# Performance work log

Hardware: AMD Instinct MI355X
Metric: run time of the kernel (lower is better)

## Reference

```python
import jax, jax.numpy as jnp
import numpy as np

HEADS = 4
K = 3  # neighborhood kernel size
EPS = 1e-5


def _nbr_idx(dim, k):
    # NATTEN semantics: window start clamped so the full k-window stays in-bounds.
    i = jnp.arange(dim)
    start = jnp.clip(i - k // 2, 0, dim - k)
    return start[:, None] + jnp.arange(k)[None, :]  # [dim, k]


def _gather_windows(t, ix, iy, iz):
    # t: [B, X, Y, Z, n, c] -> [B, X, Y, Z, K^3, n, c]
    t = t[:, ix]                 # [B, X, k, Y, Z, n, c]
    t = t[:, :, :, iy]           # [B, X, k, Y, k, Z, n, c]
    t = t[:, :, :, :, :, iz]     # [B, X, k, Y, k, Z, k, n, c]
    t = t.transpose(0, 1, 3, 5, 2, 4, 6, 7, 8)  # [B,X,Y,Z,k,k,k,n,c]
    B, X, Y, Z = t.shape[0], t.shape[1], t.shape[2], t.shape[3]
    return t.reshape(B, X, Y, Z, K * K * K, HEADS, -1)


def setup_inputs() -> dict:
    key = jax.random.key(0)
    k1, k2, k3 = jax.random.split(key, 3)
    C = 128
    x = jax.random.normal(k1, (1, C, 32, 32, 32), dtype=jnp.float32)
    ln_gamma = jnp.ones((C,), jnp.float32)
    ln_beta = jnp.zeros((C,), jnp.float32)
    qkv_w = jax.random.normal(k2, (3 * C, C), dtype=jnp.float32) * 0.02
    qkv_b = jnp.zeros((3 * C,), jnp.float32)
    proj_w = jax.random.normal(k3, (C, C), dtype=jnp.float32) * 0.02
    proj_b = jnp.zeros((C,), jnp.float32)
    return {"x": x, "ln_gamma": ln_gamma, "ln_beta": ln_beta,
            "qkv_w": qkv_w, "qkv_b": qkv_b, "proj_w": proj_w, "proj_b": proj_b}


def reference(x, ln_gamma, ln_beta, qkv_w, qkv_b, proj_w, proj_b):
    B, C, X, Y, Z = x.shape
    hd = C // HEADS
    scale = hd ** -0.5

    # permute to channels-last + LayerNorm over C
    h = x.transpose(0, 2, 3, 4, 1)  # [B,X,Y,Z,C]
    mu = jnp.mean(h, axis=-1, keepdims=True)
    var = jnp.mean(jnp.square(h - mu), axis=-1, keepdims=True)
    h = (h - mu) * jax.lax.rsqrt(var + EPS) * ln_gamma + ln_beta

    # QKV projection
    qkv = h @ qkv_w.T + qkv_b                     # [B,X,Y,Z,3C]
    q, k, v = jnp.split(qkv, 3, axis=-1)
    q = q.reshape(B, X, Y, Z, HEADS, hd)
    k = k.reshape(B, X, Y, Z, HEADS, hd)
    v = v.reshape(B, X, Y, Z, HEADS, hd)

    ix, iy, iz = _nbr_idx(X, K), _nbr_idx(Y, K), _nbr_idx(Z, K)
    k_win = _gather_windows(k, ix, iy, iz)  # [B,X,Y,Z,27,n,hd]
    v_win = _gather_windows(v, ix, iy, iz)

    attn = jnp.einsum('bxyznc,bxyzknc->bxyznk', q * scale, k_win)
    attn = jax.nn.softmax(attn, axis=-1)
    out = jnp.einsum('bxyznk,bxyzknc->bxyznc', attn, v_win)
    out = out.reshape(B, X, Y, Z, C)

    out = out @ proj_w.T + proj_b                 # output projection
    return out.transpose(0, 4, 1, 2, 3) + x      # residual, channels-first
```

## Files before the change

kernel.cpp:

```cpp
#include <hip/hip_runtime.h>

#define N_VOX 32768
#define CCH 128
#define EPSV 1e-5f

typedef __attribute__((ext_vector_type(8))) short bfrag;
typedef __attribute__((ext_vector_type(4))) float ffrag;
typedef __attribute__((ext_vector_type(2))) unsigned int u32x2;

__device__ __forceinline__ float bf2f(unsigned short u) {
    union { unsigned int i; float f; } c; c.i = ((unsigned int)u) << 16; return c.f;
}
__device__ __forceinline__ unsigned short f2bf(float f) {
    union { float f; unsigned int i; } c; c.f = f;
    unsigned int i = c.i;
    return (unsigned short)((i + 0x7FFFu + ((i >> 16) & 1u)) >> 16);
}
__device__ __forceinline__ unsigned int cvtpk(float lo, float hi) {
    unsigned int r;
    asm("v_cvt_pk_bf16_f32 %0, %1, %2" : "=v"(r) : "v"(lo), "v"(hi));
    return r;
}

__global__ __launch_bounds__(256) void ln_qkv(const float* __restrict__ x,
                                              const float* __restrict__ gamma,
                                              const float* __restrict__ beta,
                                              const float* __restrict__ w,
                                              const float* __restrict__ bias,
                                              unsigned short* __restrict__ qkv) {
    __shared__ __align__(16) unsigned short a_s[64 * 136];
    __shared__ __align__(16) unsigned short b_s[64 * 136];
    __shared__ float ps[256], pq[256];
    __shared__ float muS[64], rsS[64];
    __shared__ float g[128], bta[128];
    int t = threadIdx.x;
    int og = blockIdx.x;
    int v0 = blockIdx.y * 64;
    if (t < 128) { g[t] = gamma[t]; bta[t] = beta[t]; }
    int cq = t >> 6, v = t & 63;
    float xr[32];
    float s = 0.f, sq = 0.f;
    #pragma unroll
    for (int i = 0; i < 32; i++) {
        float val = x[(size_t)(cq * 32 + i) * N_VOX + v0 + v];
        xr[i] = val; s += val; sq += val * val;
    }
    ps[t] = s; pq[t] = sq;
    __syncthreads();
    if (t < 64) {
        float S = ps[t] + ps[t + 64] + ps[t + 128] + ps[t + 192];
        float Q = pq[t] + pq[t + 64] + pq[t + 128] + pq[t + 192];
        float mu = S * (1.0f / 128.0f);
        float var = Q * (1.0f / 128.0f) - mu * mu;
        muS[t] = mu; rsS[t] = rsqrtf(var + EPSV);
    }
    __syncthreads();
    {
        float mu = muS[v], rs = rsS[v];
        #pragma unroll
        for (int i8 = 0; i8 < 4; i8++) {
            float val[8];
            #pragma unroll
            for (int k = 0; k < 8; k++) {
                int c = cq * 32 + i8 * 8 + k;
                val[k] = (xr[i8 * 8 + k] - mu) * rs * g[c] + bta[c];
            }
            uint4 q;
            q.x = cvtpk(val[0], val[1]);
            q.y = cvtpk(val[2], val[3]);
            q.z = cvtpk(val[4], val[5]);
            q.w = cvtpk(val[6], val[7]);
            *(uint4*)&a_s[v * 136 + cq * 32 + i8 * 8] = q;
        }
    }
    __syncthreads();
    int lane = t & 63, wvi = t >> 6, m = lane & 15, quad = lane >> 4;
    bfrag areg[4];
    #pragma unroll
    for (int kk = 0; kk < 4; kk++)
        areg[kk] = *(bfrag*)&a_s[(wvi * 16 + m) * 136 + kk * 32 + quad * 8];
    for (int t0 = 0; t0 < 3; t0++) {
        int o0 = og * 192 + t0 * 64;
        {
            int r4 = t >> 4, c8 = t & 15;
            #pragma unroll
            for (int pass = 0; pass < 4; pass++) {
                int r = pass * 16 + r4;
                float4 w0 = *(const float4*)&w[(size_t)(o0 + r) * 128 + c8 * 8];
                float4 w1 = *(const float4*)&w[(size_t)(o0 + r) * 128 + c8 * 8 + 4];
                uint4 q;
                q.x = cvtpk(w0.x, w0.y);
                q.y = cvtpk(w0.z, w0.w);
                q.z = cvtpk(w1.x, w1.y);
                q.w = cvtpk(w1.z, w1.w);
                *(uint4*)&b_s[r * 136 + c8 * 8] = q;
            }
        }
        __syncthreads();
        ffrag acc[4] = {ffrag{0,0,0,0}, ffrag{0,0,0,0}, ffrag{0,0,0,0}, ffrag{0,0,0,0}};
        #pragma unroll
        for (int kk = 0; kk < 4; kk++) {
            #pragma unroll
            for (int nt = 0; nt < 4; nt++) {
                bfrag bb = *(bfrag*)&b_s[(nt * 16 + m) * 136 + kk * 32 + quad * 8];
                acc[nt] = __builtin_amdgcn_mfma_f32_16x16x32_bf16(areg[kk], bb, acc[nt], 0, 0, 0);
            }
        }
        bool isq = (o0 < 128);
        #pragma unroll
        for (int nt = 0; nt < 4; nt++) {
            int o = o0 + nt * 16 + m;
            float bs = bias[o];
            int sec = o >> 7;
            int oc = o & 127;
            unsigned short* dst = qkv + (size_t)sec * ((size_t)N_VOX * 128);
            #pragma unroll
            for (int r = 0; r < 4; r++) {
                int vg = v0 + wvi * 16 + quad * 4 + r;
                float val = acc[nt][r] + bs;
                if (isq) val *= 0.17677669529663687f;
                dst[(size_t)vg * 128 + oc] = f2bf(val);
            }
        }
        __syncthreads();
    }
}

#define VT2 100
__global__ __launch_bounds__(256) void attn_kernel(const unsigned short* __restrict__ qb,
                                                   const unsigned short* __restrict__ kb,
                                                   const unsigned short* __restrict__ vb,
                                                   unsigned short* __restrict__ ob) {
    __shared__ unsigned int vjtab[96];
    __shared__ __align__(16) unsigned int vmsk[96];
    __shared__ __align__(16) unsigned short vt[4][32 * VT2];

    int t = threadIdx.x;
    int hw = blockIdx.x;
    int bidx = (hw & 7) * 256 + (hw >> 3);
    int czi = bidx & 7, cyi = (bidx >> 3) & 15, cxi = bidx >> 7;
    int cx0 = cxi << 1, cy0 = cyi << 1, cz0 = czi << 2;
    int rx0 = min(max(cx0 - 1, 0), 28);
    int ry0 = min(max(cy0 - 1, 0), 28);
    int rz0 = min(max(cz0 - 1, 0), 26);

    if (t < 96) {
        int r = t;
        int ax = r / 24;
        int rem = r - ax * 24;
        int by = rem / 6;
        int cz = rem - by * 6;
        vjtab[t] = (unsigned)(((rx0 + ax) << 10) + ((ry0 + by) << 5) + (rz0 + cz));
        int wx0 = min(max(cx0 - 1, 0), 29) - rx0;
        int wx1 = min(cx0, 29) - rx0;
        int wy0 = min(max(cy0 - 1, 0), 29) - ry0;
        int wy1 = min(cy0, 29) - ry0;
        unsigned zn = 0;
        #pragma unroll
        for (int vz = 0; vz < 4; vz++) {
            int wz = min(max(cz0 + vz - 1, 0), 29) - rz0;
            if ((unsigned)(cz - wz) <= 2u) zn |= 1u << vz;
        }
        bool x0 = (unsigned)(ax - wx0) <= 2u;
        bool x1 = (unsigned)(ax - wx1) <= 2u;
        bool y0 = (unsigned)(by - wy0) <= 2u;
        bool y1 = (unsigned)(by - wy1) <= 2u;
        unsigned msk = 0;
        if (x0 && y0) msk |= zn;
        if (x0 && y1) msk |= zn << 4;
        if (x1 && y0) msk |= zn << 8;
        if (x1 && y1) msk |= zn << 12;
        vmsk[t] = msk;
    }
    __syncthreads();

    int wave = t >> 6, lane = t & 63;
    int hq = lane >> 4;
    int m = lane & 15;
    int ch0 = wave * 32;

    unsigned short* vts = &vt[wave][0];
    {
        const int cp = m;
        #pragma unroll
        for (int u = 0; u < 6; u++) {
            int rb = u * 16 + hq * 4;
            unsigned int j0 = vjtab[rb + 0];
            unsigned int j1 = vjtab[rb + 1];
            unsigned int j2 = vjtab[rb + 2];
            unsigned int j3 = vjtab[rb + 3];
            unsigned int d0 = *(const unsigned int*)&vb[(size_t)j0 * 128 + ch0 + cp * 2];
            unsigned int d1 = *(const unsigned int*)&vb[(size_t)j1 * 128 + ch0 + cp * 2];
            unsigned int d2 = *(const unsigned int*)&vb[(size_t)j2 * 128 + ch0 + cp * 2];
            unsigned int d3 = *(const unsigned int*)&vb[(size_t)j3 * 128 + ch0 + cp * 2];
            unsigned int lo01 = __builtin_amdgcn_perm(d1, d0, 0x05040100u);
            unsigned int lo23 = __builtin_amdgcn_perm(d3, d2, 0x05040100u);
            unsigned int hi01 = __builtin_amdgcn_perm(d1, d0, 0x07060302u);
            unsigned int hi23 = __builtin_amdgcn_perm(d3, d2, 0x07060302u);
            u32x2 wlo; wlo.x = lo01; wlo.y = lo23;
            u32x2 whi; whi.x = hi01; whi.y = hi23;
            *(u32x2*)&vts[(2 * cp) * VT2 + rb] = wlo;
            *(u32x2*)&vts[(2 * cp + 1) * VT2 + rb] = whi;
        }
    }

    int gx = cx0 + (m >> 3), gy = cy0 + ((m >> 2) & 1), gz = cz0 + (m & 3);
    int vox = (gx << 10) + (gy << 5) + gz;

    bfrag qf = *(const bfrag*)&qb[(size_t)vox * 128 + ch0 + hq * 8];
    ffrag s[6];
    #pragma unroll
    for (int f = 0; f < 6; f++) {
        unsigned int vj = vjtab[f * 16 + m];
        bfrag kf = *(const bfrag*)&kb[(size_t)vj * 128 + ch0 + hq * 8];
        s[f] = __builtin_amdgcn_mfma_f32_16x16x32_bf16(kf, qf, ffrag{0,0,0,0}, 0, 0, 0);
    }

    float mx = -1e30f;
    #pragma unroll
    for (int f = 0; f < 6; f++) {
        uint4 mk = *(const uint4*)&vmsk[f * 16 + hq * 4];
        unsigned mm[4] = {mk.x, mk.y, mk.z, mk.w};
        #pragma unroll
        for (int i = 0; i < 4; i++) {
            bool valid = (mm[i] >> m) & 1u;
            float sv = valid ? s[f][i] : -1e30f;
            s[f][i] = sv;
            mx = fmaxf(mx, sv);
        }
    }
    mx = fmaxf(mx, __shfl_xor(mx, 16));
    mx = fmaxf(mx, __shfl_xor(mx, 32));
    float sum = 0.f;
    #pragma unroll
    for (int f = 0; f < 6; f++) {
        #pragma unroll
        for (int i = 0; i < 4; i++) {
            float p = __expf(s[f][i] - mx);
            s[f][i] = p;
            sum += p;
        }
    }
    sum += __shfl_xor(sum, 16);
    sum += __shfl_xor(sum, 32);
    float inv = 1.0f / sum;

    ffrag acc0 = ffrag{0,0,0,0};
    ffrag acc1 = ffrag{0,0,0,0};
    const unsigned short* ab = &vt[wave][m * VT2 + hq * 4];
    #pragma unroll
    for (int f = 0; f < 6; f++) {
        u32x2 pb; pb.x = cvtpk(s[f][0], s[f][1]); pb.y = cvtpk(s[f][2], s[f][3]);
        u32x2 av0 = *(const u32x2*)&ab[f * 16];
        u32x2 av1 = *(const u32x2*)&ab[16 * VT2 + f * 16];
        asm("v_mfma_f32_16x16x16_bf16 %0, %1, %2, %0" : "+v"(acc0) : "v"(av0), "v"(pb));
        asm("v_mfma_f32_16x16x16_bf16 %0, %1, %2, %0" : "+v"(acc1) : "v"(av1), "v"(pb));
    }

    size_t obase = (size_t)vox * 128 + ch0 + hq * 4;
    {
        u32x2 ov;
        ov.x = cvtpk(acc0[0] * inv, acc0[1] * inv);
        ov.y = cvtpk(acc0[2] * inv, acc0[3] * inv);
        *(u32x2*)&ob[obase] = ov;
    }
    {
        u32x2 ov;
        ov.x = cvtpk(acc1[0] * inv, acc1[1] * inv);
        ov.y = cvtpk(acc1[2] * inv, acc1[3] * inv);
        *(u32x2*)&ob[obase + 16] = ov;
    }
}

__global__ __launch_bounds__(256) void proj_gemm(const unsigned short* __restrict__ a,
                                                 const float* __restrict__ w,
                                                 const float* __restrict__ bias,
                                                 const float* __restrict__ xres,
                                                 float* __restrict__ out) {
    __shared__ __align__(16) unsigned short a_s[64 * 136];
    __shared__ __align__(16) unsigned short b_s[64 * 136];
    int t = threadIdx.x;
    int m0 = blockIdx.x * 64, o0 = blockIdx.y * 64;
    {
        int r4 = t >> 4, c8 = t & 15;
        #pragma unroll
        for (int pass = 0; pass < 4; pass++) {
            int r = pass * 16 + r4;
            *(uint4*)&a_s[r * 136 + c8 * 8] =
                *(const uint4*)&a[(size_t)(m0 + r) * 128 + c8 * 8];
            float4 w0 = *(const float4*)&w[(size_t)(o0 + r) * 128 + c8 * 8];
            float4 w1 = *(const float4*)&w[(size_t)(o0 + r) * 128 + c8 * 8 + 4];
            uint4 q;
            q.x = cvtpk(w0.x, w0.y);
            q.y = cvtpk(w0.z, w0.w);
            q.z = cvtpk(w1.x, w1.y);
            q.w = cvtpk(w1.z, w1.w);
            *(uint4*)&b_s[r * 136 + c8 * 8] = q;
        }
    }
    __syncthreads();
    int wvi = t >> 6, lane = t & 63, m = lane & 15, quad = lane >> 4;
    ffrag acc[4] = {ffrag{0,0,0,0}, ffrag{0,0,0,0}, ffrag{0,0,0,0}, ffrag{0,0,0,0}};
    #pragma unroll
    for (int kk = 0; kk < 4; kk++) {
        bfrag av = *(bfrag*)&a_s[(wvi * 16 + m) * 136 + kk * 32 + quad * 8];
        #pragma unroll
        for (int nt = 0; nt < 4; nt++) {
            bfrag bb = *(bfrag*)&b_s[(nt * 16 + m) * 136 + kk * 32 + quad * 8];
            acc[nt] = __builtin_amdgcn_mfma_f32_16x16x32_bf16(av, bb, acc[nt], 0, 0, 0);
        }
    }
    #pragma unroll
    for (int nt = 0; nt < 4; nt++) {
        int o = o0 + nt * 16 + m;
        float bs = bias[o];
        int vg = m0 + wvi * 16 + quad * 4;
        float4 r = *(const float4*)&xres[(size_t)o * N_VOX + vg];
        float4 ov;
        ov.x = acc[nt][0] + bs + r.x;
        ov.y = acc[nt][1] + bs + r.y;
        ov.z = acc[nt][2] + bs + r.z;
        ov.w = acc[nt][3] + bs + r.w;
        *(float4*)&out[(size_t)o * N_VOX + vg] = ov;
    }
}

extern "C" void kernel_launch(void* const* d_in, const int* in_sizes, int n_in,
                              void* d_out, int out_size, void* d_ws, size_t ws_size,
                              hipStream_t stream) {
    const float* x      = (const float*)d_in[0];
    const float* gamma  = (const float*)d_in[1];
    const float* beta   = (const float*)d_in[2];
    const float* qkv_w  = (const float*)d_in[3];
    const float* qkv_b  = (const float*)d_in[4];
    const float* proj_w = (const float*)d_in[5];
    const float* proj_b = (const float*)d_in[6];
    float* out = (float*)d_out;

    unsigned short* qkv  = (unsigned short*)d_ws;
    unsigned short* attn = (unsigned short*)((char*)d_ws + (24u << 20));

    hipLaunchKernelGGL(ln_qkv, dim3(2, 512), dim3(256), 0, stream,
                       x, gamma, beta, qkv_w, qkv_b, qkv);
    const unsigned short* qb = qkv;
    const unsigned short* kb = qkv + (size_t)N_VOX * 128;
    const unsigned short* vb = qkv + (size_t)2 * N_VOX * 128;
    hipLaunchKernelGGL(attn_kernel, dim3(2048), dim3(256), 0, stream, qb, kb, vb, attn);
    hipLaunchKernelGGL(proj_gemm, dim3(512, 2), dim3(256), 0, stream, attn, proj_w, proj_b, x, out);
}
```

Before: 112.6 us.

## Fuse output projection into attention kernel and pre-convert weights to bf16

Adds a small kernel that converts the QKV and projection weights to bf16 once per call. The QKV GEMM then loads bf16 weights directly instead of converting fp32 in every block. The output projection, bias and residual are moved into the attention kernel's epilogue. Attention outputs are staged in LDS and multiplied against projection weights read from global memory, which removes the intermediate attention buffer round-trip and one launch. The cost is an extra launch and per-element scalar output stores that are strided by channel rather than vectorized.

New measurement: 132.2 us. 17.4% more time.

```diff
diff --git a/kernel.cpp b/kernel.cpp
--- a/kernel.cpp
+++ b/kernel.cpp
@@ -8,9 +8,6 @@
 typedef __attribute__((ext_vector_type(4))) float ffrag;
 typedef __attribute__((ext_vector_type(2))) unsigned int u32x2;
 
-__device__ __forceinline__ float bf2f(unsigned short u) {
-    union { unsigned int i; float f; } c; c.i = ((unsigned int)u) << 16; return c.f;
-}
 __device__ __forceinline__ unsigned short f2bf(float f) {
     union { float f; unsigned int i; } c; c.f = f;
     unsigned int i = c.i;
@@ -22,10 +19,27 @@
     return r;
 }
 
+__global__ __launch_bounds__(256) void wconv(const float* __restrict__ qkv_w,
+                                             const float* __restrict__ proj_w,
+                                             unsigned short* __restrict__ wq,
+                                             unsigned short* __restrict__ wp) {
+    int i = blockIdx.x * 256 + threadIdx.x;
+    if (i < 12288) {
+        float4 v = ((const float4*)qkv_w)[i];
+        u32x2 o; o.x = cvtpk(v.x, v.y); o.y = cvtpk(v.z, v.w);
+        *(u32x2*)&wq[i * 4] = o;
+    } else {
+        int j = i - 12288;
+        float4 v = ((const float4*)proj_w)[j];
+        u32x2 o; o.x = cvtpk(v.x, v.y); o.y = cvtpk(v.z, v.w);
+        *(u32x2*)&wp[j * 4] = o;
+    }
+}
+
 __global__ __launch_bounds__(256) void ln_qkv(const float* __restrict__ x,
                                               const float* __restrict__ gamma,
                                               const float* __restrict__ beta,
-                                              const float* __restrict__ w,
+                                              const unsigned short* __restrict__ wq,
                                               const float* __restrict__ bias,
                                               unsigned short* __restrict__ qkv) {
     __shared__ __align__(16) unsigned short a_s[64 * 136];
@@ -86,14 +100,8 @@
             #pragma unroll
             for (int pass = 0; pass < 4; pass++) {
                 int r = pass * 16 + r4;
-                float4 w0 = *(const float4*)&w[(size_t)(o0 + r) * 128 + c8 * 8];
-                float4 w1 = *(const float4*)&w[(size_t)(o0 + r) * 128 + c8 * 8 + 4];
-                uint4 q;
-                q.x = cvtpk(w0.x, w0.y);
-                q.y = cvtpk(w0.z, w0.w);
-                q.z = cvtpk(w1.x, w1.y);
-                q.w = cvtpk(w1.z, w1.w);
-                *(uint4*)&b_s[r * 136 + c8 * 8] = q;
+                *(uint4*)&b_s[r * 136 + c8 * 8] =
+                    *(const uint4*)&wq[(size_t)(o0 + r) * 128 + c8 * 8];
             }
         }
         __syncthreads();
@@ -127,10 +135,13 @@
 }
 
 #define VT2 100
-__global__ __launch_bounds__(256) void attn_kernel(const unsigned short* __restrict__ qb,
-                                                   const unsigned short* __restrict__ kb,
-                                                   const unsigned short* __restrict__ vb,
-                                                   unsigned short* __restrict__ ob) {
+__global__ __launch_bounds__(256) void attn_proj(const unsigned short* __restrict__ qb,
+                                                 const unsigned short* __restrict__ kb,
+                                                 const unsigned short* __restrict__ vb,
+                                                 const unsigned short* __restrict__ wp,
+                                                 const float* __restrict__ pbias,
+                                                 const float* __restrict__ xres,
+                                                 float* __restrict__ out) {
     __shared__ unsigned int vjtab[96];
     __shared__ __align__(16) unsigned int vmsk[96];
     __shared__ __align__(16) unsigned short vt[4][32 * VT2];
@@ -257,71 +268,43 @@
         asm("v_mfma_f32_16x16x16_bf16 %0, %1, %2, %0" : "+v"(acc1) : "v"(av1), "v"(pb));
     }
 
-    size_t obase = (size_t)vox * 128 + ch0 + hq * 4;
+    unsigned int af0 = cvtpk(acc0[0] * inv, acc0[1] * inv);
+    unsigned int af1 = cvtpk(acc0[2] * inv, acc0[3] * inv);
+    unsigned int af2 = cvtpk(acc1[0] * inv, acc1[1] * inv);
+    unsigned int af3 = cvtpk(acc1[2] * inv, acc1[3] * inv);
+    __syncthreads();
+    unsigned int* os = (unsigned int*)&vt[0][0];
     {
-        u32x2 ov;
-        ov.x = cvtpk(acc0[0] * inv, acc0[1] * inv);
-        ov.y = cvtpk(acc0[2] * inv, acc0[3] * inv);
-        *(u32x2*)&ob[obase] = ov;
-    }
-    {
-        u32x2 ov;
-        ov.x = cvtpk(acc1[0] * inv, acc1[1] * inv);
-        ov.y = cvtpk(acc1[2] * inv, acc1[3] * inv);
-        *(u32x2*)&ob[obase + 16] = ov;
-    }
-}
-
-__global__ __launch_bounds__(256) void proj_gemm(const unsigned short* __restrict__ a,
-                                                 const float* __restrict__ w,
-                                                 const float* __restrict__ bias,
-                                                 const float* __restrict__ xres,
-                                                 float* __restrict__ out) {
-    __shared__ __align__(16) unsigned short a_s[64 * 136];
-    __shared__ __align__(16) unsigned short b_s[64 * 136];
-    int t = threadIdx.x;
-    int m0 = blockIdx.x * 64, o0 = blockIdx.y * 64;
-    {
-        int r4 = t >> 4, c8 = t & 15;
-        #pragma unroll
-        for (int pass = 0; pass < 4; pass++) {
-            int r = pass * 16 + r4;
-            *(uint4*)&a_s[r * 136 + c8 * 8] =
-                *(const uint4*)&a[(size_t)(m0 + r) * 128 + c8 * 8];
-            float4 w0 = *(const float4*)&w[(size_t)(o0 + r) * 128 + c8 * 8];
-            float4 w1 = *(const float4*)&w[(size_t)(o0 + r) * 128 + c8 * 8 + 4];
-            uint4 q;
-            q.x = cvtpk(w0.x, w0.y);
-            q.y = cvtpk(w0.z, w0.w);
-            q.z = cvtpk(w1.x, w1.y);
-            q.w = cvtpk(w1.z, w1.w);
-            *(uint4*)&b_s[r * 136 + c8 * 8] = q;
-        }
-    }
-    __syncthreads();
-    int wvi = t >> 6, lane = t & 63, m = lane & 15, quad = lane >> 4;
-    ffrag acc[4] = {ffrag{0,0,0,0}, ffrag{0,0,0,0}, ffrag{0,0,0,0}, ffrag{0,0,0,0}};
-    #pragma unroll
-    for (int kk = 0; kk < 4; kk++) {
-        bfrag av = *(bfrag*)&a_s[(wvi * 16 + m) * 136 + kk * 32 + quad * 8];
-        #pragma unroll
-        for (int nt = 0; nt < 4; nt++) {
-            bfrag bb = *(bfrag*)&b_s[(nt * 16 + m) * 136 + kk * 32 + quad * 8];
-            acc[nt] = __builtin_amdgcn_mfma_f32_16x16x32_bf16(av, bb, acc[nt], 0, 0, 0);
-        }
-    }
-    #pragma unroll
-    for (int nt = 0; nt < 4; nt++) {
-        int o = o0 + nt * 16 + m;
-        float bs = bias[o];
-        int vg = m0 + wvi * 16 + quad * 4;
-        float4 r = *(const float4*)&xres[(size_t)o * N_VOX + vg];
-        float4 ov;
-        ov.x = acc[nt][0] + bs + r.x;
-        ov.y = acc[nt][1] + bs + r.y;
-        ov.z = acc[nt][2] + bs + r.z;
-        ov.w = acc[nt][3] + bs + r.w;
-        *(float4*)&out[(size_t)o * N_VOX + vg] = ov;
+        unsigned int* osl = os + (wave * 64 + lane) * 6;
+        u32x2 w0; w0.x = af0; w0.y = af1;
+        u32x2 w1; w1.x = af2; w1.y = af3;
+        *(u32x2*)osl = w0;
+        *(u32x2*)(osl + 2) = w1;
+    }
+    __syncthreads();
+
+    ffrag pacc0 = ffrag{0,0,0,0};
+    ffrag pacc1 = ffrag{0,0,0,0};
+    int cA = wave * 32;
+    int cB = cA + 16;
+    #pragma unroll
+    for (int cb2 = 0; cb2 < 8; cb2++) {
+        int wsrc = cb2 >> 1, half = cb2 & 1;
+        u32x2 bfr = *(const u32x2*)(os + (wsrc * 64 + hq * 16 + m) * 6 + half * 2);
+        u32x2 awA = *(const u32x2*)&wp[(size_t)(cA + m) * 128 + cb2 * 16 + hq * 4];
+        u32x2 awB = *(const u32x2*)&wp[(size_t)(cB + m) * 128 + cb2 * 16 + hq * 4];
+        asm("v_mfma_f32_16x16x16_bf16 %0, %1, %2, %0" : "+v"(pacc0) : "v"(awA), "v"(bfr));
+        asm("v_mfma_f32_16x16x16_bf16 %0, %1, %2, %0" : "+v"(pacc1) : "v"(awB), "v"(bfr));
+    }
+
+    #pragma unroll
+    for (int r = 0; r < 4; r++) {
+        int c0 = cA + hq * 4 + r;
+        int c1 = cB + hq * 4 + r;
+        size_t i0 = (size_t)c0 * N_VOX + vox;
+        size_t i1 = (size_t)c1 * N_VOX + vox;
+        out[i0] = pacc0[r] + pbias[c0] + xres[i0];
+        out[i1] = pacc1[r] + pbias[c1] + xres[i1];
     }
 }
 
@@ -337,14 +320,16 @@
     const float* proj_b = (const float*)d_in[6];
     float* out = (float*)d_out;
 
-    unsigned short* qkv  = (unsigned short*)d_ws;
-    unsigned short* attn = (unsigned short*)((char*)d_ws + (24u << 20));
-
+    unsigned short* qkv = (unsigned short*)d_ws;
+    unsigned short* wq  = (unsigned short*)((char*)d_ws + (24u << 20));
+    unsigned short* wpb = wq + 384 * 128;
+
+    hipLaunchKernelGGL(wconv, dim3(64), dim3(256), 0, stream, qkv_w, proj_w, wq, wpb);
     hipLaunchKernelGGL(ln_qkv, dim3(2, 512), dim3(256), 0, stream,
-                       x, gamma, beta, qkv_w, qkv_b, qkv);
+                       x, gamma, beta, wq, qkv_b, qkv);
     const unsigned short* qb = qkv;
     const unsigned short* kb = qkv + (size_t)N_VOX * 128;
     const unsigned short* vb = qkv + (size_t)2 * N_VOX * 128;
-    hipLaunchKernelGGL(attn_kernel, dim3(2048), dim3(256), 0, stream, qb, kb, vb, attn);
-    hipLaunchKernelGGL(proj_gemm, dim3(512, 2), dim3(256), 0, stream, attn, proj_w, proj_b, x, out);
-}
+    hipLaunchKernelGGL(attn_proj, dim3(2048), dim3(256), 0, stream,
+                       qb, kb, vb, wpb, proj_b, x, out);
+}
```
